# Kernel tuning notes

Hardware: AMD Instinct MI355X
Metric: run time of the kernel (lower is better)

Reference implementation:

```python
import jax, jax.numpy as jnp
import numpy as np

B, N_IN, N_MID, N_OUT = 262144, 64, 128, 32


def setup_inputs() -> dict:
    key = jax.random.key(0)
    kx, k1, kb1, k2, kb2 = jax.random.split(key, 5)
    v1 = 1.0 / np.sqrt(N_IN)   # per-synapse init range sqrt(1/len(dendrites))
    v2 = 1.0 / np.sqrt(N_MID)
    return {
        "x": jax.random.normal(kx, (B, N_IN), dtype=jnp.float32),
        "W1": jax.random.uniform(k1, (N_IN, N_MID), minval=-v1, maxval=v1, dtype=jnp.float32),
        "b1": jnp.zeros((N_MID,), dtype=jnp.float32),  # obtain_float_parameter inits biases to 0.0
        "W2": jax.random.uniform(k2, (N_MID, N_OUT), minval=-v2, maxval=v2, dtype=jnp.float32),
        "b2": jnp.zeros((N_OUT,), dtype=jnp.float32),
    }


def reference(x, W1, b1, W2, b2):
    # RegularNeuron: sum_i k_ij * x_i + b_j, then ReLU
    h = jax.nn.relu(x @ W1 + b1)          # [B, N_MID]
    # Output DestinationNeuron: sum_j k_jo * h_j + b_o, no activation
    y = h @ W2 + b2                        # [B, N_OUT]
    return y
```

## Files before the change

### kernel.cpp

```cpp
#include <hip/hip_runtime.h>
#include <hip/hip_bf16.h>

#define B_ROWS 262144
#define N_TILES (B_ROWS / 16)

typedef short short8 __attribute__((ext_vector_type(8)));
typedef float f32x4 __attribute__((ext_vector_type(4)));

__device__ inline short f2bf(float f) {
    __hip_bfloat16 h = __float2bfloat16(f);
    return __builtin_bit_cast(short, h);
}

__global__ __launch_bounds__(256, 2) void livenet_mlp(
    const float* __restrict__ x, const float* __restrict__ W1,
    const float* __restrict__ b1, const float* __restrict__ W2,
    const float* __restrict__ b2, float* __restrict__ y) {
    __shared__ __align__(16) short w1s[128 * 64];
    __shared__ __align__(16) short w2s[32 * 128];

    const int tid  = threadIdx.x;
    const int wid  = tid >> 6;
    const int lane = tid & 63;
    const int g    = lane >> 4;
    const int q    = lane & 15;

#pragma unroll
    for (int p = 0; p < 8; ++p) {
        const int idx = p * 1024 + tid * 4;
        f32x4 v = *(const f32x4*)(W1 + idx);
        const int r = idx >> 7, c = idx & 127;
#pragma unroll
        for (int e = 0; e < 4; ++e) {
            const int ce = c + e;
            w1s[ce * 64 + (((r >> 3) ^ (ce & 7)) * 8) + (r & 7)] = f2bf(v[e]);
        }
    }
#pragma unroll
    for (int p = 0; p < 4; ++p) {
        const int idx = p * 1024 + tid * 4;
        f32x4 v = *(const f32x4*)(W2 + idx);
        const int r = idx >> 5, c = idx & 31;
#pragma unroll
        for (int e = 0; e < 4; ++e) {
            const int ce = c + e;
            w2s[ce * 128 + (((r >> 3) ^ (2 * (ce & 7))) * 8) + (r & 7)] = f2bf(v[e]);
        }
    }
    __syncthreads();

    short8 w1f[2][8];
#pragma unroll
    for (int ks = 0; ks < 2; ++ks)
#pragma unroll
        for (int n = 0; n < 8; ++n) {
            const int pc = 32 * (n & 3) + 8 * (q >> 2) + 4 * (n >> 2) + (q & 3);
            w1f[ks][n] = *(const short8*)&w1s[pc * 64 + ((4 * ks + g) ^ (pc & 7)) * 8];
        }
    short8 w2f[4][2];
#pragma unroll
    for (int ks = 0; ks < 4; ++ks)
#pragma unroll
        for (int n = 0; n < 2; ++n) {
            const int c = n * 16 + q;
            w2f[ks][n] = *(const short8*)&w2s[c * 128 + ((4 * ks + g) ^ (2 * (q & 7))) * 8];
        }
    f32x4 binit1[8], binit2[2];
#pragma unroll
    for (int n = 0; n < 8; ++n)
        binit1[n] = *(const f32x4*)(b1 + 32 * (n & 3) + 8 * g + 4 * (n >> 2));
#pragma unroll
    for (int n = 0; n < 2; ++n)
        binit2[n] = *(const f32x4*)(b2 + n * 16 + 4 * g);

    const int gwave = blockIdx.x * 4 + wid;
    const int S     = gridDim.x * 4;
    const float* xl = x + (size_t)q * 64 + g * 8;

    f32x4 cur0, cur1, cur2, cur3, nxt0, nxt1, nxt2, nxt3;
    {
        const f32x4* p = (const f32x4*)(xl + (size_t)gwave * 1024);
        cur0 = p[0]; cur1 = p[1]; cur2 = p[8]; cur3 = p[9];
    }

    for (int tile = gwave; tile < N_TILES; tile += S) {
        const int tn = tile + S;
        if (tn < N_TILES) {
            const f32x4* p = (const f32x4*)(xl + (size_t)tn * 1024);
            nxt0 = p[0]; nxt1 = p[1]; nxt2 = p[8]; nxt3 = p[9];
        }

        const int row0 = tile * 16;

        short8 a0, a1;
        {
            short8 v;
            v[0] = f2bf(cur0[0]); v[1] = f2bf(cur0[1]); v[2] = f2bf(cur0[2]); v[3] = f2bf(cur0[3]);
            v[4] = f2bf(cur1[0]); v[5] = f2bf(cur1[1]); v[6] = f2bf(cur1[2]); v[7] = f2bf(cur1[3]);
            a0 = v;
            v[0] = f2bf(cur2[0]); v[1] = f2bf(cur2[1]); v[2] = f2bf(cur2[2]); v[3] = f2bf(cur2[3]);
            v[4] = f2bf(cur3[0]); v[5] = f2bf(cur3[1]); v[6] = f2bf(cur3[2]); v[7] = f2bf(cur3[3]);
            a1 = v;
        }

        f32x4 acc1[8];
#pragma unroll
        for (int n = 0; n < 8; ++n) {
            acc1[n] = __builtin_amdgcn_mfma_f32_16x16x32_bf16(w1f[0][n], a0, binit1[n], 0, 0, 0);
            acc1[n] = __builtin_amdgcn_mfma_f32_16x16x32_bf16(w1f[1][n], a1, acc1[n], 0, 0, 0);
        }

        short8 ha[4];
#pragma unroll
        for (int ks = 0; ks < 4; ++ks) {
            short8 v;
            v[0] = f2bf(fmaxf(acc1[ks][0], 0.0f));
            v[1] = f2bf(fmaxf(acc1[ks][1], 0.0f));
            v[2] = f2bf(fmaxf(acc1[ks][2], 0.0f));
            v[3] = f2bf(fmaxf(acc1[ks][3], 0.0f));
            v[4] = f2bf(fmaxf(acc1[ks + 4][0], 0.0f));
            v[5] = f2bf(fmaxf(acc1[ks + 4][1], 0.0f));
            v[6] = f2bf(fmaxf(acc1[ks + 4][2], 0.0f));
            v[7] = f2bf(fmaxf(acc1[ks + 4][3], 0.0f));
            ha[ks] = v;
        }

        f32x4 acc2[2];
#pragma unroll
        for (int n = 0; n < 2; ++n) {
            acc2[n] = __builtin_amdgcn_mfma_f32_16x16x32_bf16(w2f[0][n], ha[0], binit2[n], 0, 0, 0);
#pragma unroll
            for (int ks = 1; ks < 4; ++ks)
                acc2[n] = __builtin_amdgcn_mfma_f32_16x16x32_bf16(w2f[ks][n], ha[ks], acc2[n], 0, 0, 0);
        }

#pragma unroll
        for (int n = 0; n < 2; ++n)
            __builtin_nontemporal_store(
                acc2[n], (f32x4*)(y + (size_t)(row0 + q) * 32 + n * 16 + 4 * g));

        cur0 = nxt0; cur1 = nxt1; cur2 = nxt2; cur3 = nxt3;
    }
}

extern "C" void kernel_launch(void* const* d_in, const int* in_sizes, int n_in,
                              void* d_out, int out_size, void* d_ws, size_t ws_size,
                              hipStream_t stream) {
    const float* x  = (const float*)d_in[0];
    const float* W1 = (const float*)d_in[1];
    const float* b1 = (const float*)d_in[2];
    const float* W2 = (const float*)d_in[3];
    const float* b2 = (const float*)d_in[4];
    float* y = (float*)d_out;

    const int blocks = 512;
    livenet_mlp<<<blocks, 256, 0, stream>>>(x, W1, b1, W2, b2, y);
}
```

Before: 24.32 us.

## Read weight fragments from LDS per tile instead of holding them in registers

Weight fragments are no longer cached in VGPRs for the whole kernel. Each tile reloads them from LDS, and the LDS weights are stored twice so alternating tiles read from alternating copies. This frees registers so launch bounds and the grid can be raised to three blocks per CU. In exchange, every tile now issues many more LDS reads, and the block doubles its LDS footprint.

```diff
diff --git a/kernel.cpp b/kernel.cpp
--- a/kernel.cpp
+++ b/kernel.cpp
@@ -3,6 +3,8 @@
 
 #define B_ROWS 262144
 #define N_TILES (B_ROWS / 16)
+#define W1COPY 8192
+#define W2COPY 4096
 
 typedef short short8 __attribute__((ext_vector_type(8)));
 typedef float f32x4 __attribute__((ext_vector_type(4)));
@@ -12,12 +14,12 @@
     return __builtin_bit_cast(short, h);
 }
 
-__global__ __launch_bounds__(256, 2) void livenet_mlp(
+__global__ __launch_bounds__(256, 3) void livenet_mlp(
     const float* __restrict__ x, const float* __restrict__ W1,
     const float* __restrict__ b1, const float* __restrict__ W2,
     const float* __restrict__ b2, float* __restrict__ y) {
-    __shared__ __align__(16) short w1s[128 * 64];
-    __shared__ __align__(16) short w2s[32 * 128];
+    __shared__ __align__(16) short w1s[2 * W1COPY];
+    __shared__ __align__(16) short w2s[2 * W2COPY];
 
     const int tid  = threadIdx.x;
     const int wid  = tid >> 6;
@@ -26,45 +28,47 @@
     const int q    = lane & 15;
 
 #pragma unroll
-    for (int p = 0; p < 8; ++p) {
-        const int idx = p * 1024 + tid * 4;
-        f32x4 v = *(const f32x4*)(W1 + idx);
-        const int r = idx >> 7, c = idx & 127;
+    for (int cp = 0; cp < 2; ++cp) {
 #pragma unroll
-        for (int e = 0; e < 4; ++e) {
-            const int ce = c + e;
-            w1s[ce * 64 + (((r >> 3) ^ (ce & 7)) * 8) + (r & 7)] = f2bf(v[e]);
+        for (int p = 0; p < 8; ++p) {
+            const int idx = p * 1024 + tid * 4;
+            f32x4 v = *(const f32x4*)(W1 + idx);
+            const int r = idx >> 7, c = idx & 127;
+#pragma unroll
+            for (int e = 0; e < 4; ++e) {
+                const int ce = c + e;
+                w1s[cp * W1COPY + ce * 64 + (((r >> 3) ^ (ce & 7)) * 8) + (r & 7)] = f2bf(v[e]);
+            }
         }
-    }
 #pragma unroll
-    for (int p = 0; p < 4; ++p) {
-        const int idx = p * 1024 + tid * 4;
-        f32x4 v = *(const f32x4*)(W2 + idx);
-        const int r = idx >> 5, c = idx & 31;
+        for (int p = 0; p < 4; ++p) {
+            const int idx = p * 1024 + tid * 4;
+            f32x4 v = *(const f32x4*)(W2 + idx);
+            const int r = idx >> 5, c = idx & 31;
 #pragma unroll
-        for (int e = 0; e < 4; ++e) {
-            const int ce = c + e;
-            w2s[ce * 128 + (((r >> 3) ^ (2 * (ce & 7))) * 8) + (r & 7)] = f2bf(v[e]);
+            for (int e = 0; e < 4; ++e) {
+                const int ce = c + e;
+                w2s[cp * W2COPY + ce * 128 + (((r >> 3) ^ (2 * (ce & 7))) * 8) + (r & 7)] = f2bf(v[e]);
+            }
         }
     }
     __syncthreads();
 
-    short8 w1f[2][8];
+    int w1off[2][8];
 #pragma unroll
     for (int ks = 0; ks < 2; ++ks)
 #pragma unroll
         for (int n = 0; n < 8; ++n) {
             const int pc = 32 * (n & 3) + 8 * (q >> 2) + 4 * (n >> 2) + (q & 3);
-            w1f[ks][n] = *(const short8*)&w1s[pc * 64 + ((4 * ks + g) ^ (pc & 7)) * 8];
+            w1off[ks][n] = pc * 64 + ((4 * ks + g) ^ (pc & 7)) * 8;
         }
-    short8 w2f[4][2];
+    int w2off[4][2];
 #pragma unroll
     for (int ks = 0; ks < 4; ++ks)
 #pragma unroll
-        for (int n = 0; n < 2; ++n) {
-            const int c = n * 16 + q;
-            w2f[ks][n] = *(const short8*)&w2s[c * 128 + ((4 * ks + g) ^ (2 * (q & 7))) * 8];
-        }
+        for (int n = 0; n < 2; ++n)
+            w2off[ks][n] = (n * 16 + q) * 128 + ((4 * ks + g) ^ (2 * (q & 7))) * 8;
+
     f32x4 binit1[8], binit2[2];
 #pragma unroll
     for (int n = 0; n < 8; ++n)
@@ -83,12 +87,16 @@
         cur0 = p[0]; cur1 = p[1]; cur2 = p[8]; cur3 = p[9];
     }
 
-    for (int tile = gwave; tile < N_TILES; tile += S) {
+    int parity = 0;
+    for (int tile = gwave; tile < N_TILES; tile += S, parity ^= 1) {
         const int tn = tile + S;
         if (tn < N_TILES) {
             const f32x4* p = (const f32x4*)(xl + (size_t)tn * 1024);
             nxt0 = p[0]; nxt1 = p[1]; nxt2 = p[8]; nxt3 = p[9];
         }
+
+        const short* w1b = w1s + parity * W1COPY;
+        const short* w2b = w2s + parity * W2COPY;
 
         const int row0 = tile * 16;
 
@@ -106,8 +114,10 @@
         f32x4 acc1[8];
 #pragma unroll
         for (int n = 0; n < 8; ++n) {
-            acc1[n] = __builtin_amdgcn_mfma_f32_16x16x32_bf16(w1f[0][n], a0, binit1[n], 0, 0, 0);
-            acc1[n] = __builtin_amdgcn_mfma_f32_16x16x32_bf16(w1f[1][n], a1, acc1[n], 0, 0, 0);
+            short8 wa = *(const short8*)&w1b[w1off[0][n]];
+            short8 wb = *(const short8*)&w1b[w1off[1][n]];
+            acc1[n] = __builtin_amdgcn_mfma_f32_16x16x32_bf16(wa, a0, binit1[n], 0, 0, 0);
+            acc1[n] = __builtin_amdgcn_mfma_f32_16x16x32_bf16(wb, a1, acc1[n], 0, 0, 0);
         }
 
         short8 ha[4];
@@ -128,10 +138,12 @@
         f32x4 acc2[2];
 #pragma unroll
         for (int n = 0; n < 2; ++n) {
-            acc2[n] = __builtin_amdgcn_mfma_f32_16x16x32_bf16(w2f[0][n], ha[0], binit2[n], 0, 0, 0);
+            acc2[n] = binit2[n];
 #pragma unroll
-            for (int ks = 1; ks < 4; ++ks)
-                acc2[n] = __builtin_amdgcn_mfma_f32_16x16x32_bf16(w2f[ks][n], ha[ks], acc2[n], 0, 0, 0);
+            for (int ks = 0; ks < 4; ++ks) {
+                short8 w = *(const short8*)&w2b[w2off[ks][n]];
+                acc2[n] = __builtin_amdgcn_mfma_f32_16x16x32_bf16(w, ha[ks], acc2[n], 0, 0, 0);
+            }
         }
 
 #pragma unroll
@@ -153,6 +165,6 @@
     const float* b2 = (const float*)d_in[4];
     float* y = (float*)d_out;
 
-    const int blocks = 512;
+    const int blocks = 768;
     livenet_mlp<<<blocks, 256, 0, stream>>>(x, W1, b1, W2, b2, y);
 }
```

Measured after the change: 30.72 us. +26.3%, slower.
